# Kernel optimization log

Measured on AMD Instinct MI355X. Metric: run time of the kernel, lower is better.

## Reference

```python
import jax, jax.numpy as jnp
import numpy as np

B, T = 32, 4096
CAT, NE, HS = 128, 512, 64


def setup_inputs() -> dict:
    key = jax.random.key(0)
    ks = jax.random.split(key, 8)
    s = lambda fan_in: 1.0 / np.sqrt(fan_in)
    return {
        "x": jax.random.normal(ks[0], (B, T, NE), dtype=jnp.float32),
        "cat_emb": jax.random.normal(ks[1], (B, CAT), dtype=jnp.float32),
        # weights stored [in, out] (torch Linear weight transposed)
        "Wq": jax.random.uniform(ks[2], (CAT, HS), minval=-s(CAT), maxval=s(CAT), dtype=jnp.float32),
        "Wk": jax.random.uniform(ks[3], (NE, HS), minval=-s(NE), maxval=s(NE), dtype=jnp.float32),
        "Wv": jax.random.uniform(ks[4], (NE, HS), minval=-s(NE), maxval=s(NE), dtype=jnp.float32),
        "Wp": jax.random.uniform(ks[5], (HS, NE), minval=-s(HS), maxval=s(HS), dtype=jnp.float32),
        "gamma": jnp.ones((NE,), dtype=jnp.float32),
        "beta": jnp.zeros((NE,), dtype=jnp.float32),
    }


def reference(x, cat_emb, Wq, Wk, Wv, Wp, gamma, beta):
    # single-query cross attention: category vector attends over sequence
    q = cat_emb @ Wq                      # [B, HS]
    k = jnp.einsum("btn,nh->bth", x, Wk)  # [B, T, HS]
    v = jnp.einsum("btn,nh->bth", x, Wv)  # [B, T, HS]
    scale = 1.0 / jnp.sqrt(jnp.asarray(HS, dtype=x.dtype))
    wei = jnp.einsum("bh,bth->bt", q, k) * scale   # [B, T] scores
    wei = jax.nn.softmax(wei, axis=-1)
    out = jnp.einsum("bt,bth->bh", wei, v)         # [B, HS] attended value
    # proj + LayerNorm computed once per batch row (values are identical
    # across T since query length is 1), then broadcast to [B, T, NE]
    y = out @ Wp                                   # [B, NE]
    mu = jnp.mean(y, axis=-1, keepdims=True)
    var = jnp.mean(jnp.square(y - mu), axis=-1, keepdims=True)
    y = (y - mu) / jnp.sqrt(var + 1e-5) * gamma + beta
    return jnp.broadcast_to(y[:, None, :], (x.shape[0], x.shape[1], y.shape[-1]))
```

## Files before the change

kernel.cpp:

```cpp
#include <hip/hip_runtime.h>
#include <hip/hip_bf16.h>
#include <math.h>

#define B_   32
#define T_   4096
#define CAT_ 128
#define NE_  512
#define HS_  64

#define CHUNKS_ 32
#define ROWS_PER_BLOCK_ (T_ / CHUNKS_)
#define ROWS_PER_WAVE_  (ROWS_PER_BLOCK_ / 4)

__global__ __launch_bounds__(64) void k_kq(const float* __restrict__ cat_emb,
                                           const float* __restrict__ Wq,
                                           const float* __restrict__ Wk,
                                           float* __restrict__ kq) {
    const int b = blockIdx.x;
    const int t = threadIdx.x;
    __shared__ float sq[HS_];
    float q = 0.f;
    #pragma unroll 4
    for (int c = 0; c < CAT_; ++c) q += cat_emb[b * CAT_ + c] * Wq[c * HS_ + t];
    sq[t] = q;
    __syncthreads();
    #pragma unroll
    for (int i = 0; i < NE_ / 64; ++i) {
        const int n = i * 64 + t;
        float acc = 0.f;
        #pragma unroll 8
        for (int h = 0; h < HS_; ++h) acc += Wk[n * HS_ + h] * sq[h];
        kq[b * NE_ + n] = acc * 0.125f;
    }
}

__global__ __launch_bounds__(256) void k_pass1(const float* __restrict__ x,
                                               const float* __restrict__ kq,
                                               float* __restrict__ pm,
                                               float* __restrict__ pl,
                                               float* __restrict__ pacc) {
    const int blk   = blockIdx.x;
    const int b     = blk >> 5;
    const int chunk = blk & 31;
    const int wave  = threadIdx.x >> 6;
    const int lane  = threadIdx.x & 63;

    const float4* kq4 = (const float4*)(kq + b * NE_);
    const float4 kq0 = kq4[lane];
    const float4 kq1 = kq4[lane + 64];

    const float* xb = x + (size_t)b * T_ * NE_;
    const int t0 = chunk * ROWS_PER_BLOCK_ + wave * ROWS_PER_WAVE_;

    float m = -INFINITY, l = 0.f;
    float a00 = 0.f, a01 = 0.f, a02 = 0.f, a03 = 0.f;
    float a10 = 0.f, a11 = 0.f, a12 = 0.f, a13 = 0.f;

    for (int r = 0; r < ROWS_PER_WAVE_; ++r) {
        const float4* xr = (const float4*)(xb + (size_t)(t0 + r) * NE_);
        const float4 x0 = xr[lane];
        const float4 x1 = xr[lane + 64];
        float p = x0.x * kq0.x + x0.y * kq0.y + x0.z * kq0.z + x0.w * kq0.w
                + x1.x * kq1.x + x1.y * kq1.y + x1.z * kq1.z + x1.w * kq1.w;
        #pragma unroll
        for (int off = 32; off >= 1; off >>= 1) p += __shfl_xor(p, off, 64);
        const float nm = fmaxf(m, p);
        const float f  = __expf(m - nm);
        const float w  = __expf(p - nm);
        m = nm;
        l = l * f + w;
        a00 = a00 * f + w * x0.x;  a01 = a01 * f + w * x0.y;
        a02 = a02 * f + w * x0.z;  a03 = a03 * f + w * x0.w;
        a10 = a10 * f + w * x1.x;  a11 = a11 * f + w * x1.y;
        a12 = a12 * f + w * x1.z;  a13 = a13 * f + w * x1.w;
    }

    __shared__ float sm[4], sl[4];
    __shared__ float sacc[4 * NE_];
    if (lane == 0) { sm[wave] = m; sl[wave] = l; }
    float4* sa = (float4*)(sacc + wave * NE_);
    sa[lane]      = make_float4(a00, a01, a02, a03);
    sa[lane + 64] = make_float4(a10, a11, a12, a13);
    __syncthreads();

    const float M  = fmaxf(fmaxf(sm[0], sm[1]), fmaxf(sm[2], sm[3]));
    const float f0 = __expf(sm[0] - M), f1 = __expf(sm[1] - M);
    const float f2 = __expf(sm[2] - M), f3 = __expf(sm[3] - M);
    const int n = threadIdx.x;
    float* dst = pacc + (size_t)blk * NE_;
    dst[n]       = f0 * sacc[0 * NE_ + n]       + f1 * sacc[1 * NE_ + n]
                 + f2 * sacc[2 * NE_ + n]       + f3 * sacc[3 * NE_ + n];
    dst[n + 256] = f0 * sacc[0 * NE_ + n + 256] + f1 * sacc[1 * NE_ + n + 256]
                 + f2 * sacc[2 * NE_ + n + 256] + f3 * sacc[3 * NE_ + n + 256];
    if (threadIdx.x == 0) {
        pm[blk] = M;
        pl[blk] = f0 * sl[0] + f1 * sl[1] + f2 * sl[2] + f3 * sl[3];
    }
}

__global__ __launch_bounds__(256) void k_combine(const float* __restrict__ pm,
                                                 const float* __restrict__ pl,
                                                 const float* __restrict__ pacc,
                                                 const float* __restrict__ Wv,
                                                 const float* __restrict__ Wp,
                                                 const float* __restrict__ gamma,
                                                 const float* __restrict__ beta,
                                                 float* __restrict__ ynorm) {
    const int b   = blockIdx.x;
    const int tid = threadIdx.x;
    __shared__ float xbar[NE_];
    __shared__ float sout[HS_];
    __shared__ float red[256];

    float M = -INFINITY;
    #pragma unroll
    for (int p = 0; p < CHUNKS_; ++p) M = fmaxf(M, pm[b * CHUNKS_ + p]);
    float L = 0.f, x0 = 0.f, x1 = 0.f;
    for (int p = 0; p < CHUNKS_; ++p) {
        const float f = __expf(pm[b * CHUNKS_ + p] - M);
        L += f * pl[b * CHUNKS_ + p];
        const float* a = pacc + (size_t)(b * CHUNKS_ + p) * NE_;
        x0 += f * a[tid];
        x1 += f * a[tid + 256];
    }
    const float rL = 1.f / L;
    xbar[tid] = x0 * rL;
    xbar[tid + 256] = x1 * rL;
    __syncthreads();

    const int h = tid & 63, seg = tid >> 6;
    float o = 0.f;
    #pragma unroll 8
    for (int i = 0; i < NE_ / 4; ++i) {
        const int nn = seg * (NE_ / 4) + i;
        o += xbar[nn] * Wv[nn * HS_ + h];
    }
    red[tid] = o;
    __syncthreads();
    if (tid < 64) sout[tid] = red[tid] + red[tid + 64] + red[tid + 128] + red[tid + 192];
    __syncthreads();

    float y0 = 0.f, y1 = 0.f;
    #pragma unroll 8
    for (int hh = 0; hh < HS_; ++hh) {
        const float oh = sout[hh];
        y0 += oh * Wp[hh * NE_ + tid];
        y1 += oh * Wp[hh * NE_ + tid + 256];
    }

    red[tid] = y0 + y1;
    __syncthreads();
    for (int s = 128; s > 0; s >>= 1) { if (tid < s) red[tid] += red[tid + s]; __syncthreads(); }
    const float mu = red[0] * (1.f / NE_);
    __syncthreads();
    const float d0 = y0 - mu, d1 = y1 - mu;
    red[tid] = d0 * d0 + d1 * d1;
    __syncthreads();
    for (int s = 128; s > 0; s >>= 1) { if (tid < s) red[tid] += red[tid + s]; __syncthreads(); }
    const float rstd = rsqrtf(red[0] * (1.f / NE_) + 1e-5f);
    ynorm[b * NE_ + tid]       = d0 * rstd * gamma[tid]       + beta[tid];
    ynorm[b * NE_ + tid + 256] = d1 * rstd * gamma[tid + 256] + beta[tid + 256];
}

__global__ __launch_bounds__(256) void k_bcast(const float4* __restrict__ y4,
                                               float4* __restrict__ out4) {
    const unsigned u = blockIdx.x * 256u + threadIdx.x;
    const int n4 = u & 127;
    #pragma unroll 4
    for (int b = 0; b < B_; ++b) {
        out4[(size_t)b * (T_ * NE_ / 4) + u] = y4[(b << 7) + n4];
    }
}

extern "C" void kernel_launch(void* const* d_in, const int* in_sizes, int n_in,
                              void* d_out, int out_size, void* d_ws, size_t ws_size,
                              hipStream_t stream) {
    const float* x       = (const float*)d_in[0];
    const float* cat_emb = (const float*)d_in[1];
    const float* Wq      = (const float*)d_in[2];
    const float* Wk      = (const float*)d_in[3];
    const float* Wv      = (const float*)d_in[4];
    const float* Wp      = (const float*)d_in[5];
    const float* gamma   = (const float*)d_in[6];
    const float* beta    = (const float*)d_in[7];
    float* out = (float*)d_out;

    float* ws    = (float*)d_ws;
    float* kq    = ws;
    float* pm    = kq + B_ * NE_;
    float* pl    = pm + B_ * CHUNKS_;
    float* pacc  = pl + B_ * CHUNKS_;
    float* ynorm = pacc + (size_t)B_ * CHUNKS_ * NE_;

    k_kq<<<B_, 64, 0, stream>>>(cat_emb, Wq, Wk, kq);
    k_pass1<<<B_ * CHUNKS_, 256, 0, stream>>>(x, kq, pm, pl, pacc);
    k_combine<<<B_, 256, 0, stream>>>(pm, pl, pacc, Wv, Wp, gamma, beta, ynorm);
    k_bcast<<<(T_ * NE_ / 4) / 256, 256, 0, stream>>>((const float4*)ynorm, (float4*)out);
}
```

Before: 513.7 us.

## Fuse query/key projection into main pass and use nontemporal loads and stores

Folds the small kq kernel into the main streaming kernel, so each block recomputes q and Wk·q into shared memory. This removes one launch and the round trip of kq through global memory. x reads and output broadcast writes now use nontemporal builtins, and the broadcast kernel is reorganised so each block writes a contiguous batch segment. The cost is redundant per-block recomputation of the tiny projection (1024 blocks times a 512x64 dot pass over Wk).

Measured after the change: 469.9 us. -8.5%, faster.

```diff
diff --git a/kernel.cpp b/kernel.cpp
--- a/kernel.cpp
+++ b/kernel.cpp
@@ -9,92 +9,106 @@
 #define HS_  64
 
 #define CHUNKS_ 32
-#define ROWS_PER_BLOCK_ (T_ / CHUNKS_)
-#define ROWS_PER_WAVE_  (ROWS_PER_BLOCK_ / 4)
-
-__global__ __launch_bounds__(64) void k_kq(const float* __restrict__ cat_emb,
-                                           const float* __restrict__ Wq,
-                                           const float* __restrict__ Wk,
-                                           float* __restrict__ kq) {
-    const int b = blockIdx.x;
-    const int t = threadIdx.x;
-    __shared__ float sq[HS_];
-    float q = 0.f;
-    #pragma unroll 4
-    for (int c = 0; c < CAT_; ++c) q += cat_emb[b * CAT_ + c] * Wq[c * HS_ + t];
-    sq[t] = q;
-    __syncthreads();
-    #pragma unroll
-    for (int i = 0; i < NE_ / 64; ++i) {
-        const int n = i * 64 + t;
-        float acc = 0.f;
-        #pragma unroll 8
-        for (int h = 0; h < HS_; ++h) acc += Wk[n * HS_ + h] * sq[h];
-        kq[b * NE_ + n] = acc * 0.125f;
-    }
-}
-
-__global__ __launch_bounds__(256) void k_pass1(const float* __restrict__ x,
-                                               const float* __restrict__ kq,
-                                               float* __restrict__ pm,
-                                               float* __restrict__ pl,
-                                               float* __restrict__ pacc) {
+#define RPB_ (T_ / CHUNKS_)
+#define RPW_ (RPB_ / 4)
+
+typedef float f4 __attribute__((ext_vector_type(4)));
+
+__global__ __launch_bounds__(256, 4) void k_main(
+    const float* __restrict__ x, const float* __restrict__ cat_emb,
+    const float* __restrict__ Wq, const float* __restrict__ Wk,
+    float* __restrict__ pm, float* __restrict__ pl, float* __restrict__ pacc)
+{
     const int blk   = blockIdx.x;
     const int b     = blk >> 5;
     const int chunk = blk & 31;
-    const int wave  = threadIdx.x >> 6;
-    const int lane  = threadIdx.x & 63;
-
-    const float4* kq4 = (const float4*)(kq + b * NE_);
-    const float4 kq0 = kq4[lane];
-    const float4 kq1 = kq4[lane + 64];
-
-    const float* xb = x + (size_t)b * T_ * NE_;
-    const int t0 = chunk * ROWS_PER_BLOCK_ + wave * ROWS_PER_WAVE_;
-
-    float m = -INFINITY, l = 0.f;
-    float a00 = 0.f, a01 = 0.f, a02 = 0.f, a03 = 0.f;
-    float a10 = 0.f, a11 = 0.f, a12 = 0.f, a13 = 0.f;
-
-    for (int r = 0; r < ROWS_PER_WAVE_; ++r) {
-        const float4* xr = (const float4*)(xb + (size_t)(t0 + r) * NE_);
-        const float4 x0 = xr[lane];
-        const float4 x1 = xr[lane + 64];
-        float p = x0.x * kq0.x + x0.y * kq0.y + x0.z * kq0.z + x0.w * kq0.w
-                + x1.x * kq1.x + x1.y * kq1.y + x1.z * kq1.z + x1.w * kq1.w;
+    const int tid   = threadIdx.x;
+    const int wave  = tid >> 6;
+    const int lane  = tid & 63;
+
+    __shared__ float sq[HS_];
+    __shared__ float skq[NE_];
+    __shared__ float red[256];
+    __shared__ float sacc[4 * NE_];
+    __shared__ float smw[4], slw[4];
+
+    {
+        const int h = tid & 63, cq = tid >> 6;
+        float qp = 0.f;
+        #pragma unroll 8
+        for (int c = cq * 32; c < cq * 32 + 32; ++c)
+            qp += cat_emb[b * CAT_ + c] * Wq[c * HS_ + h];
+        red[tid] = qp;
+        __syncthreads();
+        if (tid < 64) sq[tid] = red[tid] + red[tid + 64] + red[tid + 128] + red[tid + 192];
+        __syncthreads();
+        const f4* Wk4 = (const f4*)Wk;
+        const f4* sq4 = (const f4*)sq;
         #pragma unroll
-        for (int off = 32; off >= 1; off >>= 1) p += __shfl_xor(p, off, 64);
-        const float nm = fmaxf(m, p);
-        const float f  = __expf(m - nm);
-        const float w  = __expf(p - nm);
-        m = nm;
-        l = l * f + w;
-        a00 = a00 * f + w * x0.x;  a01 = a01 * f + w * x0.y;
-        a02 = a02 * f + w * x0.z;  a03 = a03 * f + w * x0.w;
-        a10 = a10 * f + w * x1.x;  a11 = a11 * f + w * x1.y;
-        a12 = a12 * f + w * x1.z;  a13 = a13 * f + w * x1.w;
-    }
-
-    __shared__ float sm[4], sl[4];
-    __shared__ float sacc[4 * NE_];
-    if (lane == 0) { sm[wave] = m; sl[wave] = l; }
-    float4* sa = (float4*)(sacc + wave * NE_);
-    sa[lane]      = make_float4(a00, a01, a02, a03);
-    sa[lane + 64] = make_float4(a10, a11, a12, a13);
-    __syncthreads();
-
-    const float M  = fmaxf(fmaxf(sm[0], sm[1]), fmaxf(sm[2], sm[3]));
-    const float f0 = __expf(sm[0] - M), f1 = __expf(sm[1] - M);
-    const float f2 = __expf(sm[2] - M), f3 = __expf(sm[3] - M);
-    const int n = threadIdx.x;
-    float* dst = pacc + (size_t)blk * NE_;
-    dst[n]       = f0 * sacc[0 * NE_ + n]       + f1 * sacc[1 * NE_ + n]
-                 + f2 * sacc[2 * NE_ + n]       + f3 * sacc[3 * NE_ + n];
-    dst[n + 256] = f0 * sacc[0 * NE_ + n + 256] + f1 * sacc[1 * NE_ + n + 256]
-                 + f2 * sacc[2 * NE_ + n + 256] + f3 * sacc[3 * NE_ + n + 256];
-    if (threadIdx.x == 0) {
-        pm[blk] = M;
-        pl[blk] = f0 * sl[0] + f1 * sl[1] + f2 * sl[2] + f3 * sl[3];
+        for (int half = 0; half < 2; ++half) {
+            const int n = tid + half * 256;
+            float acc = 0.f;
+            #pragma unroll
+            for (int i = 0; i < HS_ / 4; ++i) {
+                const f4 w = Wk4[n * (HS_ / 4) + i];
+                const f4 s = sq4[i];
+                acc += w.x * s.x + w.y * s.y + w.z * s.z + w.w * s.w;
+            }
+            skq[n] = acc * 0.125f;
+        }
+        __syncthreads();
+    }
+
+    {
+        const f4* kq4 = (const f4*)skq;
+        const f4 kq0 = kq4[lane];
+        const f4 kq1 = kq4[lane + 64];
+        const float* xb = x + (size_t)b * T_ * NE_;
+        const int t0 = chunk * RPB_ + wave * RPW_;
+
+        float m = -INFINITY, l = 0.f;
+        float a00 = 0.f, a01 = 0.f, a02 = 0.f, a03 = 0.f;
+        float a10 = 0.f, a11 = 0.f, a12 = 0.f, a13 = 0.f;
+
+        for (int r = 0; r < RPW_; ++r) {
+            const f4* xr = (const f4*)(xb + (size_t)(t0 + r) * NE_);
+            const f4 x0 = __builtin_nontemporal_load(&xr[lane]);
+            const f4 x1 = __builtin_nontemporal_load(&xr[lane + 64]);
+            float p = x0.x * kq0.x + x0.y * kq0.y + x0.z * kq0.z + x0.w * kq0.w
+                    + x1.x * kq1.x + x1.y * kq1.y + x1.z * kq1.z + x1.w * kq1.w;
+            #pragma unroll
+            for (int off = 32; off >= 1; off >>= 1) p += __shfl_xor(p, off, 64);
+            const float nm = fmaxf(m, p);
+            const float f  = __expf(m - nm);
+            const float w  = __expf(p - nm);
+            m = nm;
+            l = l * f + w;
+            a00 = a00 * f + w * x0.x;  a01 = a01 * f + w * x0.y;
+            a02 = a02 * f + w * x0.z;  a03 = a03 * f + w * x0.w;
+            a10 = a10 * f + w * x1.x;  a11 = a11 * f + w * x1.y;
+            a12 = a12 * f + w * x1.z;  a13 = a13 * f + w * x1.w;
+        }
+
+        if (lane == 0) { smw[wave] = m; slw[wave] = l; }
+        f4* sa = (f4*)(sacc + wave * NE_);
+        f4 v0; v0.x = a00; v0.y = a01; v0.z = a02; v0.w = a03;
+        f4 v1; v1.x = a10; v1.y = a11; v1.z = a12; v1.w = a13;
+        sa[lane]      = v0;
+        sa[lane + 64] = v1;
+        __syncthreads();
+
+        const float Mb = fmaxf(fmaxf(smw[0], smw[1]), fmaxf(smw[2], smw[3]));
+        const float f0 = __expf(smw[0] - Mb), f1 = __expf(smw[1] - Mb);
+        const float f2 = __expf(smw[2] - Mb), f3 = __expf(smw[3] - Mb);
+        float* dst = pacc + (size_t)blk * NE_;
+        dst[tid]       = f0 * sacc[tid]               + f1 * sacc[NE_ + tid]
+                       + f2 * sacc[2 * NE_ + tid]     + f3 * sacc[3 * NE_ + tid];
+        dst[tid + 256] = f0 * sacc[tid + 256]         + f1 * sacc[NE_ + tid + 256]
+                       + f2 * sacc[2 * NE_ + tid + 256] + f3 * sacc[3 * NE_ + tid + 256];
+        if (tid == 0) {
+            pm[blk] = Mb;
+            pl[blk] = f0 * slw[0] + f1 * slw[1] + f2 * slw[2] + f3 * slw[3];
+        }
     }
 }
 
@@ -162,13 +176,18 @@
     ynorm[b * NE_ + tid + 256] = d1 * rstd * gamma[tid + 256] + beta[tid + 256];
 }
 
-__global__ __launch_bounds__(256) void k_bcast(const float4* __restrict__ y4,
-                                               float4* __restrict__ out4) {
-    const unsigned u = blockIdx.x * 256u + threadIdx.x;
-    const int n4 = u & 127;
-    #pragma unroll 4
-    for (int b = 0; b < B_; ++b) {
-        out4[(size_t)b * (T_ * NE_ / 4) + u] = y4[(b << 7) + n4];
+__global__ __launch_bounds__(256) void k_bcast(const f4* __restrict__ yn4,
+                                               f4* __restrict__ out4) {
+    const int blk = blockIdx.x;
+    const int b   = blk >> 6;
+    const int seg = blk & 63;
+    const int tid = threadIdx.x;
+    const f4 v = yn4[(b << 7) + (tid & 127)];
+    const size_t base = ((size_t)b * T_ + (size_t)seg * 64) * (NE_ / 4);
+    f4* p = out4 + base + tid;
+    #pragma unroll 8
+    for (int i = 0; i < 32; ++i) {
+        __builtin_nontemporal_store(v, p + (size_t)i * 256);
     }
 }
 
@@ -186,14 +205,12 @@
     float* out = (float*)d_out;
 
     float* ws    = (float*)d_ws;
-    float* kq    = ws;
-    float* pm    = kq + B_ * NE_;
+    float* pm    = ws;
     float* pl    = pm + B_ * CHUNKS_;
     float* pacc  = pl + B_ * CHUNKS_;
     float* ynorm = pacc + (size_t)B_ * CHUNKS_ * NE_;
 
-    k_kq<<<B_, 64, 0, stream>>>(cat_emb, Wq, Wk, kq);
-    k_pass1<<<B_ * CHUNKS_, 256, 0, stream>>>(x, kq, pm, pl, pacc);
+    k_main<<<B_ * CHUNKS_, 256, 0, stream>>>(x, cat_emb, Wq, Wk, pm, pl, pacc);
     k_combine<<<B_, 256, 0, stream>>>(pm, pl, pacc, Wv, Wp, gamma, beta, ynorm);
-    k_bcast<<<(T_ * NE_ / 4) / 256, 256, 0, stream>>>((const float4*)ynorm, (float4*)out);
-}
+    k_bcast<<<2048, 256, 0, stream>>>((const f4*)ynorm, (f4*)out);
+}
```
